# Kernel optimization log

Measured on AMD Instinct MI355X. Metric: run time of the kernel, lower is better.

The kernel has to match this reference:

```python
import jax, jax.numpy as jnp
import numpy as np

N, E, B = 50000, 800000, 512
IN, H, OUT = 128, 64, 32
BN_EPS = 1e-5


def setup_inputs() -> dict:
    key = jax.random.key(0)
    ks = jax.random.split(key, 32)
    inp = {}
    inp["x"] = jax.random.normal(ks[0], (N, IN), dtype=jnp.float32)
    inp["edge_index"] = jax.random.randint(ks[1], (2, E), 0, N, dtype=jnp.int64)
    inp["batch"] = jnp.sort(jax.random.randint(ks[2], (N,), 0, B, dtype=jnp.int64))
    inp["batch_size"] = B
    # GINConv MLP params: Linear(cin,H) -> BN(H) -> ReLU -> Linear(H,H)
    cins = [IN, H, H]
    ki = 3
    for i, cin in enumerate(cins):
        inp[f"c{i}_W1"] = jax.random.normal(ks[ki], (cin, H), dtype=jnp.float32) / np.sqrt(cin); ki += 1
        inp[f"c{i}_b1"] = jnp.zeros((H,), jnp.float32)
        inp[f"c{i}_g1"] = jnp.ones((H,), jnp.float32)
        inp[f"c{i}_bt1"] = jnp.zeros((H,), jnp.float32)
        inp[f"c{i}_W2"] = jax.random.normal(ks[ki], (H, H), dtype=jnp.float32) / np.sqrt(H); ki += 1
        inp[f"c{i}_b2"] = jnp.zeros((H,), jnp.float32)
    # final MLP (norm=None): Linear(H,H) -> ReLU -> [dropout, eval: identity] -> Linear(H,OUT)
    inp["f_W1"] = jax.random.normal(ks[ki], (H, H), dtype=jnp.float32) / np.sqrt(H); ki += 1
    inp["f_b1"] = jnp.zeros((H,), jnp.float32)
    inp["f_W2"] = jax.random.normal(ks[ki], (H, OUT), dtype=jnp.float32) / np.sqrt(H)
    inp["f_b2"] = jnp.zeros((OUT,), jnp.float32)
    return inp


def _bn(h, g, bt):
    # BatchNorm1d, training-mode statistics (biased variance), eps=1e-5
    mean = h.mean(axis=0)
    var = ((h - mean) ** 2).mean(axis=0)
    return g * (h - mean) * jax.lax.rsqrt(var + BN_EPS) + bt


def _gin_conv(x, src, dst, W1, b1, g1, bt1, W2, b2):
    # sum-aggregate neighbor features: agg[i] = sum_{(j->i)} x[j]
    agg = jax.ops.segment_sum(x[src], dst, num_segments=N)  # [N,H_in]
    h = x + agg  # (1+eps)*x + agg, eps=0
    h = jax.nn.relu(_bn(h @ W1 + b1, g1, bt1))
    return h @ W2 + b2


def reference(x, edge_index, batch, batch_size,
              c0_W1, c0_b1, c0_g1, c0_bt1, c0_W2, c0_b2,
              c1_W1, c1_b1, c1_g1, c1_bt1, c1_W2, c1_b2,
              c2_W1, c2_b1, c2_g1, c2_bt1, c2_W2, c2_b2,
              f_W1, f_b1, f_W2, f_b2):
    src, dst = edge_index[0], edge_index[1]
    convs = [(c0_W1, c0_b1, c0_g1, c0_bt1, c0_W2, c0_b2),
             (c1_W1, c1_b1, c1_g1, c1_bt1, c1_W2, c1_b2),
             (c2_W1, c2_b1, c2_g1, c2_bt1, c2_W2, c2_b2)]
    for p in convs:
        x = jax.nn.relu(_gin_conv(x, src, dst, *p))
    # global_add_pool over graph ids
    pooled = jax.ops.segment_sum(x, batch, num_segments=batch_size)  # [B,H]
    h = jax.nn.relu(pooled @ f_W1 + f_b1)  # dropout=0.5 skipped (eval mode)
    return h @ f_W2 + f_b2  # [B,OUT]
```

## Files before the change

### kernel.cpp

```cpp
#include <hip/hip_runtime.h>
#include <hip/hip_fp16.h>

#define NN 50000
#define EE 800000
#define BB 512
#define DIN 128
#define HH 64
#define DOUT 32
#define BN_EPS 1e-5f
#define SCAN_BLOCKS 196
#define GATHER_BLOCKS 2048

template <int CIN>
__global__ __launch_bounds__(256) void proj_kernel(const float* __restrict__ X,
                                                   const float* __restrict__ W,
                                                   __half2* __restrict__ Qh)
{
    __shared__ float sW[CIN * 64];
    __shared__ float sX[16 * CIN];
    const int tid = threadIdx.x;
    const int row0 = blockIdx.x * 16;

    for (int i = tid; i < CIN * 16; i += 256)
        ((float4*)sW)[i] = ((const float4*)W)[i];
    const float* Xb = X + (size_t)row0 * CIN;
    for (int i = tid; i < 16 * CIN / 4; i += 256)
        ((float4*)sX)[i] = ((const float4*)Xb)[i];
    __syncthreads();

    const int col2 = tid & 31;
    const int rg   = tid >> 5;
    float2 acc0 = {0.f, 0.f};
    float2 acc1 = {0.f, 0.f};
    const float* x0p = &sX[(rg * 2 + 0) * CIN];
    const float* x1p = &sX[(rg * 2 + 1) * CIN];
#pragma unroll 4
    for (int k = 0; k < CIN; ++k) {
        const float2 w = *(const float2*)&sW[k * 64 + col2 * 2];
        const float x0 = x0p[k];
        const float x1 = x1p[k];
        acc0.x = fmaf(x0, w.x, acc0.x);
        acc0.y = fmaf(x0, w.y, acc0.y);
        acc1.x = fmaf(x1, w.x, acc1.x);
        acc1.y = fmaf(x1, w.y, acc1.y);
    }
    const int r0 = row0 + rg * 2;
    Qh[(size_t)(r0 + 0) * 32 + col2] = __floats2half2_rn(acc0.x, acc0.y);
    Qh[(size_t)(r0 + 1) * 32 + col2] = __floats2half2_rn(acc1.x, acc1.y);
}

__global__ __launch_bounds__(256) void hist_rank_kernel(const int* __restrict__ dst,
                                                        int* __restrict__ deg,
                                                        unsigned short* __restrict__ rank)
{
    const int e = blockIdx.x * 256 + threadIdx.x;
    rank[e] = (unsigned short)atomicAdd(&deg[dst[e]], 1);
}

__global__ __launch_bounds__(256) void scanA_kernel(const int* __restrict__ deg,
                                                    int* __restrict__ offs,
                                                    int* __restrict__ blockSums)
{
    __shared__ int s[256];
    const int t = threadIdx.x;
    const int i = blockIdx.x * 256 + t;
    const int v = (i < NN) ? deg[i] : 0;
    s[t] = v;
    __syncthreads();
    for (int off = 1; off < 256; off <<= 1) {
        const int a = (t >= off) ? s[t - off] : 0;
        __syncthreads();
        s[t] += a;
        __syncthreads();
    }
    if (i < NN) offs[i] = s[t] - v;
    if (t == 255) blockSums[blockIdx.x] = s[255];
}

__global__ __launch_bounds__(256) void scanB_kernel(const int* __restrict__ blockSums,
                                                    int* __restrict__ blockOff)
{
    __shared__ int s[256];
    const int t = threadIdx.x;
    const int v = (t < SCAN_BLOCKS) ? blockSums[t] : 0;
    s[t] = v;
    __syncthreads();
    for (int off = 1; off < 256; off <<= 1) {
        const int a = (t >= off) ? s[t - off] : 0;
        __syncthreads();
        s[t] += a;
        __syncthreads();
    }
    if (t < SCAN_BLOCKS) blockOff[t] = s[t] - v;
}

__global__ __launch_bounds__(256) void scanC_kernel(int* __restrict__ offs,
                                                    const int* __restrict__ blockOff,
                                                    float* __restrict__ statsbuf,
                                                    float* __restrict__ pooled,
                                                    unsigned int* __restrict__ qzero)
{
    const int i = blockIdx.x * 256 + threadIdx.x;
    if (i < NN) offs[i] += blockOff[blockIdx.x];
    if (i == 0) offs[NN] = EE;
    if (i < 384) statsbuf[i] = 0.f;
    if (i < BB * 64) pooled[i] = 0.f;
    if (blockIdx.x == 1 && threadIdx.x < 32) qzero[threadIdx.x] = 0u;
}

__global__ __launch_bounds__(256) void scatter_kernel(const int* __restrict__ src,
                                                      const int* __restrict__ dst,
                                                      const unsigned short* __restrict__ rank,
                                                      const int* __restrict__ offs,
                                                      unsigned short* __restrict__ srcSorted)
{
    const int e = blockIdx.x * 256 + threadIdx.x;
    const int pos = offs[dst[e]] + (int)rank[e];
    srcSorted[pos] = (unsigned short)src[e];
}

__global__ __launch_bounds__(256) void gather_kernel(const __half2* __restrict__ Qh,
                                                     const int* __restrict__ offs,
                                                     const unsigned short* __restrict__ srcSorted,
                                                     const float* __restrict__ b1,
                                                     float* __restrict__ Z,
                                                     float* __restrict__ sums,
                                                     float* __restrict__ sumsq)
{
    const int tid  = threadIdx.x;
    const int lane = tid & 63;
    const int wid  = tid >> 6;
    const int colq = lane & 15;
    const int grp  = lane >> 4;
    const uint2* Qr = (const uint2*)Qh;
    const float4 bb = ((const float4*)b1)[colq];

    float sa0 = 0.f, sa1 = 0.f, sa2 = 0.f, sa3 = 0.f;
    float ta0 = 0.f, ta1 = 0.f, ta2 = 0.f, ta3 = 0.f;

    for (int node = blockIdx.x * 4 + wid; node < NN; node += GATHER_BLOCKS * 4) {
        const int o0 = offs[node];
        const int o1 = offs[node + 1];
        float a0 = 0.f, a1 = 0.f, a2 = 0.f, a3 = 0.f;
        int j = o0;
        while (o1 - j > 48) {
            int idx[12];
#pragma unroll
            for (int k = 0; k < 12; ++k) idx[k] = srcSorted[j + k * 4 + grp];
            uint2 r[12];
#pragma unroll
            for (int k = 0; k < 12; ++k) r[k] = Qr[(size_t)idx[k] * 16 + colq];
#pragma unroll
            for (int k = 0; k < 12; ++k) {
                float2 p;
                p = __half22float2(*(const __half2*)&r[k].x); a0 += p.x; a1 += p.y;
                p = __half22float2(*(const __half2*)&r[k].y); a2 += p.x; a3 += p.y;
            }
            j += 48;
        }
        {
            int idx[12];
#pragma unroll
            for (int k = 0; k < 12; ++k) {
                const int p = j + k * 4 + grp;
                const int v = srcSorted[p];
                idx[k] = (p < o1) ? v : NN;
            }
            uint2 r[12];
#pragma unroll
            for (int k = 0; k < 12; ++k) r[k] = Qr[(size_t)idx[k] * 16 + colq];
#pragma unroll
            for (int k = 0; k < 12; ++k) {
                float2 p;
                p = __half22float2(*(const __half2*)&r[k].x); a0 += p.x; a1 += p.y;
                p = __half22float2(*(const __half2*)&r[k].y); a2 += p.x; a3 += p.y;
            }
        }
        a0 += __shfl_xor(a0, 16); a1 += __shfl_xor(a1, 16);
        a2 += __shfl_xor(a2, 16); a3 += __shfl_xor(a3, 16);
        a0 += __shfl_xor(a0, 32); a1 += __shfl_xor(a1, 32);
        a2 += __shfl_xor(a2, 32); a3 += __shfl_xor(a3, 32);
        if (grp == 0) {
            const uint2 sr = Qr[(size_t)node * 16 + colq];
            float2 p;
            p = __half22float2(*(const __half2*)&sr.x); a0 += p.x + bb.x; a1 += p.y + bb.y;
            p = __half22float2(*(const __half2*)&sr.y); a2 += p.x + bb.z; a3 += p.y + bb.w;
            float4 zv = {a0, a1, a2, a3};
            ((float4*)Z)[(size_t)node * 16 + colq] = zv;
            sa0 += a0; sa1 += a1; sa2 += a2; sa3 += a3;
            ta0 += a0 * a0; ta1 += a1 * a1; ta2 += a2 * a2; ta3 += a3 * a3;
        }
    }

    __shared__ float red[4][16][8];
    if (grp == 0) {
        float* rp = red[wid][colq];
        rp[0] = sa0; rp[1] = sa1; rp[2] = sa2; rp[3] = sa3;
        rp[4] = ta0; rp[5] = ta1; rp[6] = ta2; rp[7] = ta3;
    }
    __syncthreads();
    if (tid < 128) {
        const int cq = tid >> 3;
        const int k  = tid & 7;
        const float v = red[0][cq][k] + red[1][cq][k] + red[2][cq][k] + red[3][cq][k];
        float* dstp = (k < 4) ? &sums[cq * 4 + k] : &sumsq[cq * 4 + (k - 4)];
        atomicAdd(dstp, v);
    }
}

template <bool POOL>
__global__ __launch_bounds__(256) void gemm2_kernel(const float* __restrict__ Z,
                                                    const float* __restrict__ sums,
                                                    const float* __restrict__ sumsq,
                                                    const float* __restrict__ g1,
                                                    const float* __restrict__ bt1,
                                                    const float* __restrict__ W2,
                                                    const float* __restrict__ b2,
                                                    const int* __restrict__ batch,
                                                    float* __restrict__ out)
{
    __shared__ float sW[64 * 64];
    __shared__ float sH[16 * 64];
    __shared__ float sScale[64];
    __shared__ float sShift[64];
    const int tid = threadIdx.x;
    const int row0 = blockIdx.x * 16;

    if (tid < 64) {
        const float inv_n = 1.0f / (float)NN;
        const float mean = sums[tid] * inv_n;
        const float var = fmaxf(sumsq[tid] * inv_n - mean * mean, 0.f);
        const float sc = g1[tid] * rsqrtf(var + BN_EPS);
        sScale[tid] = sc;
        sShift[tid] = bt1[tid] - mean * sc;
    }
    for (int i = tid; i < 64 * 16; i += 256)
        ((float4*)sW)[i] = ((const float4*)W2)[i];
    __syncthreads();

    const float4* Zb = (const float4*)(Z + (size_t)row0 * 64);
    {
        const int i = tid;
        const float4 z = Zb[i];
        const int c4 = i & 15;
        const float4 sc = ((const float4*)sScale)[c4];
        const float4 sh = ((const float4*)sShift)[c4];
        float4 h;
        h.x = fmaxf(fmaf(z.x, sc.x, sh.x), 0.f);
        h.y = fmaxf(fmaf(z.y, sc.y, sh.y), 0.f);
        h.z = fmaxf(fmaf(z.z, sc.z, sh.z), 0.f);
        h.w = fmaxf(fmaf(z.w, sc.w, sh.w), 0.f);
        ((float4*)sH)[i] = h;
    }
    __syncthreads();

    const int col = tid & 63;
    const int r0  = tid >> 6;
    const float bc = b2[col];
    float acc[4] = {bc, bc, bc, bc};
    for (int k = 0; k < 64; k += 4) {
        const float w0 = sW[(k + 0) * 64 + col];
        const float w1 = sW[(k + 1) * 64 + col];
        const float w2 = sW[(k + 2) * 64 + col];
        const float w3 = sW[(k + 3) * 64 + col];
#pragma unroll
        for (int rr = 0; rr < 4; ++rr) {
            const float4 hv = *(const float4*)&sH[(r0 + rr * 4) * 64 + k];
            acc[rr] = fmaf(hv.x, w0, acc[rr]);
            acc[rr] = fmaf(hv.y, w1, acc[rr]);
            acc[rr] = fmaf(hv.z, w2, acc[rr]);
            acc[rr] = fmaf(hv.w, w3, acc[rr]);
        }
    }
#pragma unroll
    for (int rr = 0; rr < 4; ++rr) {
        const int row = row0 + r0 + rr * 4;
        const float v = fmaxf(acc[rr], 0.f);
        if (POOL) {
            atomicAdd(&out[(size_t)batch[row] * 64 + col], v);
        } else {
            out[(size_t)row * 64 + col] = v;
        }
    }
}

__global__ __launch_bounds__(256) void final_mlp(const float* __restrict__ P,
                                                 const float* __restrict__ W1,
                                                 const float* __restrict__ b1,
                                                 const float* __restrict__ W2,
                                                 const float* __restrict__ b2,
                                                 float* __restrict__ out)
{
    __shared__ float sW1[64 * 64];
    __shared__ float sW2[64 * 32];
    __shared__ float sH[4 * 64];
    const int tid = threadIdx.x;
    const int row0 = blockIdx.x * 4;

    for (int i = tid; i < 1024; i += 256) ((float4*)sW1)[i] = ((const float4*)W1)[i];
    for (int i = tid; i < 512; i += 256) ((float4*)sW2)[i] = ((const float4*)W2)[i];
    __syncthreads();

    const int col = tid & 63;
    const int r = tid >> 6;
    float acc = b1[col];
    const float* prow = P + (size_t)(row0 + r) * 64;
    for (int k = 0; k < 64; ++k) acc = fmaf(prow[k], sW1[k * 64 + col], acc);
    sH[r * 64 + col] = fmaxf(acc, 0.f);
    __syncthreads();

    if (tid < 128) {
        const int c = tid & 31;
        const int r2 = tid >> 5;
        float a2 = b2[c];
        for (int k = 0; k < 64; ++k) a2 = fmaf(sH[r2 * 64 + k], sW2[k * 32 + c], a2);
        out[(size_t)(row0 + r2) * 32 + c] = a2;
    }
}

extern "C" void kernel_launch(void* const* d_in, const int* in_sizes, int n_in,
                              void* d_out, int out_size, void* d_ws, size_t ws_size,
                              hipStream_t stream)
{
    const float* x   = (const float*)d_in[0];
    const int* ei    = (const int*)d_in[1];
    const int* batch = (const int*)d_in[2];
    const float* cW1[3] = {(const float*)d_in[4],  (const float*)d_in[10], (const float*)d_in[16]};
    const float* cb1[3] = {(const float*)d_in[5],  (const float*)d_in[11], (const float*)d_in[17]};
    const float* cg1[3] = {(const float*)d_in[6],  (const float*)d_in[12], (const float*)d_in[18]};
    const float* cbt[3] = {(const float*)d_in[7],  (const float*)d_in[13], (const float*)d_in[19]};
    const float* cW2[3] = {(const float*)d_in[8],  (const float*)d_in[14], (const float*)d_in[20]};
    const float* cb2[3] = {(const float*)d_in[9],  (const float*)d_in[15], (const float*)d_in[21]};
    const float* fW1 = (const float*)d_in[22];
    const float* fb1 = (const float*)d_in[23];
    const float* fW2 = (const float*)d_in[24];
    const float* fb2 = (const float*)d_in[25];
    float* out = (float*)d_out;

    float* bufX     = (float*)d_ws;
    __half2* Qh     = (__half2*)(bufX + (size_t)NN * 64);
    float* pooled   = (float*)(Qh + (size_t)(NN + 1) * 32);
    float* statsbuf = pooled + (size_t)BB * 64;
    int* deg        = (int*)(statsbuf + 384);
    int* offs       = deg + NN;
    int* blockSums  = offs + (NN + 1);
    int* blockOff   = blockSums + 256;
    unsigned short* rank      = (unsigned short*)(blockOff + 256);
    unsigned short* srcSorted = rank + EE;

    const int* esrc = ei;
    const int* edst = ei + EE;

    const int gemm_blocks = NN / 16;
    const int edge_blocks = EE / 256;

    hipMemsetAsync(deg, 0, NN * sizeof(int), stream);
    hist_rank_kernel<<<edge_blocks, 256, 0, stream>>>(edst, deg, rank);
    scanA_kernel<<<SCAN_BLOCKS, 256, 0, stream>>>(deg, offs, blockSums);
    scanB_kernel<<<1, 256, 0, stream>>>(blockSums, blockOff);
    scanC_kernel<<<SCAN_BLOCKS, 256, 0, stream>>>(offs, blockOff, statsbuf, pooled,
                                                  (unsigned int*)(Qh + (size_t)NN * 32));
    scatter_kernel<<<edge_blocks, 256, 0, stream>>>(esrc, edst, rank, offs, srcSorted);

    for (int layer = 0; layer < 3; ++layer) {
        float* sums  = statsbuf + layer * 128;
        float* sumsq = sums + 64;

        if (layer == 0)
            proj_kernel<DIN><<<gemm_blocks, 256, 0, stream>>>(x, cW1[0], Qh);
        else
            proj_kernel<HH><<<gemm_blocks, 256, 0, stream>>>(bufX, cW1[layer], Qh);

        gather_kernel<<<GATHER_BLOCKS, 256, 0, stream>>>(Qh, offs, srcSorted, cb1[layer],
                                                         bufX, sums, sumsq);

        if (layer < 2) {
            gemm2_kernel<false><<<gemm_blocks, 256, 0, stream>>>(bufX, sums, sumsq, cg1[layer],
                                                                 cbt[layer], cW2[layer], cb2[layer],
                                                                 nullptr, bufX);
        } else {
            gemm2_kernel<true><<<gemm_blocks, 256, 0, stream>>>(bufX, sums, sumsq, cg1[layer],
                                                                cbt[layer], cW2[layer], cb2[layer],
                                                                batch, pooled);
        }
    }

    final_mlp<<<BB / 4, 256, 0, stream>>>(pooled, fW1, fb1, fW2, fb2, out);
}
```

Measured before the change: 382.4 us.

## Pad CSR neighbor lists to multiples of sixteen for branch-free vectorized gather

Each node's neighbor list is padded to at least 16 entries, rounded up to a multiple of 16, and filled with a sentinel index that points to a zeroed Q row. This lets the gather load indices as aligned uint4 vectors and drop the per-element bounds checks. The gather is also remapped so each wave handles a node with two 32-lane halves, each lane covering one half2 column. The cost is a larger index buffer, an extra fill kernel, and wasted gathers on padding entries for low-degree nodes.

```diff
diff --git a/kernel.cpp b/kernel.cpp
--- a/kernel.cpp
+++ b/kernel.cpp
@@ -10,6 +10,7 @@
 #define BN_EPS 1e-5f
 #define SCAN_BLOCKS 196
 #define GATHER_BLOCKS 2048
+#define PADMAX (16 * NN + EE + 64)
 
 template <int CIN>
 __global__ __launch_bounds__(256) void proj_kernel(const float* __restrict__ X,
@@ -49,6 +50,12 @@
     Qh[(size_t)(r0 + 1) * 32 + col2] = __floats2half2_rn(acc1.x, acc1.y);
 }
 
+__global__ __launch_bounds__(256) void fill_kernel(unsigned int* __restrict__ dstw)
+{
+    const int i = blockIdx.x * 256 + threadIdx.x;
+    if (i < PADMAX / 2) dstw[i] = 0xC350C350u;
+}
+
 __global__ __launch_bounds__(256) void hist_rank_kernel(const int* __restrict__ dst,
                                                         int* __restrict__ deg,
                                                         unsigned short* __restrict__ rank)
@@ -58,13 +65,17 @@
 }
 
 __global__ __launch_bounds__(256) void scanA_kernel(const int* __restrict__ deg,
-                                                    int* __restrict__ offs,
+                                                    int* __restrict__ poffs,
                                                     int* __restrict__ blockSums)
 {
     __shared__ int s[256];
     const int t = threadIdx.x;
     const int i = blockIdx.x * 256 + t;
-    const int v = (i < NN) ? deg[i] : 0;
+    int v = 0;
+    if (i < NN) {
+        const int d = deg[i];
+        v = (d <= 16) ? 16 : ((d + 15) & ~15);
+    }
     s[t] = v;
     __syncthreads();
     for (int off = 1; off < 256; off <<= 1) {
@@ -73,12 +84,13 @@
         s[t] += a;
         __syncthreads();
     }
-    if (i < NN) offs[i] = s[t] - v;
+    if (i < NN) poffs[i] = s[t] - v;
     if (t == 255) blockSums[blockIdx.x] = s[255];
 }
 
 __global__ __launch_bounds__(256) void scanB_kernel(const int* __restrict__ blockSums,
-                                                    int* __restrict__ blockOff)
+                                                    int* __restrict__ blockOff,
+                                                    int* __restrict__ poffs)
 {
     __shared__ int s[256];
     const int t = threadIdx.x;
@@ -92,17 +104,17 @@
         __syncthreads();
     }
     if (t < SCAN_BLOCKS) blockOff[t] = s[t] - v;
-}
-
-__global__ __launch_bounds__(256) void scanC_kernel(int* __restrict__ offs,
+    if (t == SCAN_BLOCKS - 1) poffs[NN] = s[t];
+}
+
+__global__ __launch_bounds__(256) void scanC_kernel(int* __restrict__ poffs,
                                                     const int* __restrict__ blockOff,
                                                     float* __restrict__ statsbuf,
                                                     float* __restrict__ pooled,
                                                     unsigned int* __restrict__ qzero)
 {
     const int i = blockIdx.x * 256 + threadIdx.x;
-    if (i < NN) offs[i] += blockOff[blockIdx.x];
-    if (i == 0) offs[NN] = EE;
+    if (i < NN) poffs[i] += blockOff[blockIdx.x];
     if (i < 384) statsbuf[i] = 0.f;
     if (i < BB * 64) pooled[i] = 0.f;
     if (blockIdx.x == 1 && threadIdx.x < 32) qzero[threadIdx.x] = 0u;
@@ -111,99 +123,122 @@
 __global__ __launch_bounds__(256) void scatter_kernel(const int* __restrict__ src,
                                                       const int* __restrict__ dst,
                                                       const unsigned short* __restrict__ rank,
-                                                      const int* __restrict__ offs,
-                                                      unsigned short* __restrict__ srcSorted)
+                                                      const int* __restrict__ poffs,
+                                                      unsigned short* __restrict__ srcPadded)
 {
     const int e = blockIdx.x * 256 + threadIdx.x;
-    const int pos = offs[dst[e]] + (int)rank[e];
-    srcSorted[pos] = (unsigned short)src[e];
+    const int pos = poffs[dst[e]] + (int)rank[e];
+    srcPadded[pos] = (unsigned short)src[e];
 }
 
 __global__ __launch_bounds__(256) void gather_kernel(const __half2* __restrict__ Qh,
-                                                     const int* __restrict__ offs,
-                                                     const unsigned short* __restrict__ srcSorted,
+                                                     const int* __restrict__ poffs,
+                                                     const unsigned short* __restrict__ srcPadded,
                                                      const float* __restrict__ b1,
                                                      float* __restrict__ Z,
                                                      float* __restrict__ sums,
                                                      float* __restrict__ sumsq)
 {
-    const int tid  = threadIdx.x;
-    const int lane = tid & 63;
-    const int wid  = tid >> 6;
-    const int colq = lane & 15;
-    const int grp  = lane >> 4;
-    const uint2* Qr = (const uint2*)Qh;
-    const float4 bb = ((const float4*)b1)[colq];
-
-    float sa0 = 0.f, sa1 = 0.f, sa2 = 0.f, sa3 = 0.f;
-    float ta0 = 0.f, ta1 = 0.f, ta2 = 0.f, ta3 = 0.f;
+    const int tid   = threadIdx.x;
+    const int lane  = tid & 63;
+    const int wid   = tid >> 6;
+    const int c     = lane & 31;
+    const int grp   = lane >> 5;
+    const int shamt = grp << 4;
+    const uint* Qd  = (const uint*)Qh;
+    const float2 bb = ((const float2*)b1)[c];
+
+    float2 sa = {0.f, 0.f};
+    float2 ta = {0.f, 0.f};
 
     for (int node = blockIdx.x * 4 + wid; node < NN; node += GATHER_BLOCKS * 4) {
-        const int o0 = offs[node];
-        const int o1 = offs[node + 1];
-        float a0 = 0.f, a1 = 0.f, a2 = 0.f, a3 = 0.f;
-        int j = o0;
-        while (o1 - j > 48) {
-            int idx[12];
-#pragma unroll
-            for (int k = 0; k < 12; ++k) idx[k] = srcSorted[j + k * 4 + grp];
-            uint2 r[12];
-#pragma unroll
-            for (int k = 0; k < 12; ++k) r[k] = Qr[(size_t)idx[k] * 16 + colq];
-#pragma unroll
-            for (int k = 0; k < 12; ++k) {
-                float2 p;
-                p = __half22float2(*(const __half2*)&r[k].x); a0 += p.x; a1 += p.y;
-                p = __half22float2(*(const __half2*)&r[k].y); a2 += p.x; a3 += p.y;
+        const int p0 = poffs[node];
+        const int p1 = poffs[node + 1];
+        const bool two = (p1 - p0) > 16;
+
+        const uint4 ia = *(const uint4*)(srcPadded + p0);
+        const uint4 ib = *(const uint4*)(srcPadded + p0 + 8);
+        uint4 ia2, ib2;
+        if (two) {
+            ia2 = *(const uint4*)(srcPadded + p0 + 16);
+            ib2 = *(const uint4*)(srcPadded + p0 + 24);
+        }
+        const uint sr = Qd[(size_t)node * 32 + c];
+
+        uint r[16];
+#pragma unroll
+        for (int k = 0; k < 4; ++k) {
+            r[k]     = Qd[(size_t)(((&ia.x)[k] >> shamt) & 0xffffu) * 32 + c];
+            r[4 + k] = Qd[(size_t)(((&ib.x)[k] >> shamt) & 0xffffu) * 32 + c];
+        }
+        if (two) {
+#pragma unroll
+            for (int k = 0; k < 4; ++k) {
+                r[8 + k]  = Qd[(size_t)(((&ia2.x)[k] >> shamt) & 0xffffu) * 32 + c];
+                r[12 + k] = Qd[(size_t)(((&ib2.x)[k] >> shamt) & 0xffffu) * 32 + c];
             }
-            j += 48;
-        }
-        {
-            int idx[12];
-#pragma unroll
-            for (int k = 0; k < 12; ++k) {
-                const int p = j + k * 4 + grp;
-                const int v = srcSorted[p];
-                idx[k] = (p < o1) ? v : NN;
+        }
+
+        float2 acc = {0.f, 0.f};
+#pragma unroll
+        for (int k = 0; k < 8; ++k) {
+            const float2 p = __half22float2(*(const __half2*)&r[k]);
+            acc.x += p.x;
+            acc.y += p.y;
+        }
+        if (two) {
+#pragma unroll
+            for (int k = 8; k < 16; ++k) {
+                const float2 p = __half22float2(*(const __half2*)&r[k]);
+                acc.x += p.x;
+                acc.y += p.y;
             }
-            uint2 r[12];
-#pragma unroll
-            for (int k = 0; k < 12; ++k) r[k] = Qr[(size_t)idx[k] * 16 + colq];
-#pragma unroll
-            for (int k = 0; k < 12; ++k) {
-                float2 p;
-                p = __half22float2(*(const __half2*)&r[k].x); a0 += p.x; a1 += p.y;
-                p = __half22float2(*(const __half2*)&r[k].y); a2 += p.x; a3 += p.y;
+        }
+        for (int j = p0 + 32; j < p1; j += 16) {
+            const uint4 ja = *(const uint4*)(srcPadded + j);
+            const uint4 jb = *(const uint4*)(srcPadded + j + 8);
+            uint rr[8];
+#pragma unroll
+            for (int k = 0; k < 4; ++k) {
+                rr[k]     = Qd[(size_t)(((&ja.x)[k] >> shamt) & 0xffffu) * 32 + c];
+                rr[4 + k] = Qd[(size_t)(((&jb.x)[k] >> shamt) & 0xffffu) * 32 + c];
             }
-        }
-        a0 += __shfl_xor(a0, 16); a1 += __shfl_xor(a1, 16);
-        a2 += __shfl_xor(a2, 16); a3 += __shfl_xor(a3, 16);
-        a0 += __shfl_xor(a0, 32); a1 += __shfl_xor(a1, 32);
-        a2 += __shfl_xor(a2, 32); a3 += __shfl_xor(a3, 32);
+#pragma unroll
+            for (int k = 0; k < 8; ++k) {
+                const float2 p = __half22float2(*(const __half2*)&rr[k]);
+                acc.x += p.x;
+                acc.y += p.y;
+            }
+        }
+
+        acc.x += __shfl_xor(acc.x, 32);
+        acc.y += __shfl_xor(acc.y, 32);
+
         if (grp == 0) {
-            const uint2 sr = Qr[(size_t)node * 16 + colq];
-            float2 p;
-            p = __half22float2(*(const __half2*)&sr.x); a0 += p.x + bb.x; a1 += p.y + bb.y;
-            p = __half22float2(*(const __half2*)&sr.y); a2 += p.x + bb.z; a3 += p.y + bb.w;
-            float4 zv = {a0, a1, a2, a3};
-            ((float4*)Z)[(size_t)node * 16 + colq] = zv;
-            sa0 += a0; sa1 += a1; sa2 += a2; sa3 += a3;
-            ta0 += a0 * a0; ta1 += a1 * a1; ta2 += a2 * a2; ta3 += a3 * a3;
-        }
-    }
-
-    __shared__ float red[4][16][8];
+            const float2 p = __half22float2(*(const __half2*)&sr);
+            acc.x += p.x + bb.x;
+            acc.y += p.y + bb.y;
+            ((float2*)Z)[(size_t)node * 32 + c] = acc;
+            sa.x += acc.x; sa.y += acc.y;
+            ta.x += acc.x * acc.x; ta.y += acc.y * acc.y;
+        }
+    }
+
+    __shared__ float red[4][32][4];
     if (grp == 0) {
-        float* rp = red[wid][colq];
-        rp[0] = sa0; rp[1] = sa1; rp[2] = sa2; rp[3] = sa3;
-        rp[4] = ta0; rp[5] = ta1; rp[6] = ta2; rp[7] = ta3;
+        float* rp = red[wid][c];
+        rp[0] = sa.x; rp[1] = sa.y; rp[2] = ta.x; rp[3] = ta.y;
     }
     __syncthreads();
     if (tid < 128) {
-        const int cq = tid >> 3;
-        const int k  = tid & 7;
-        const float v = red[0][cq][k] + red[1][cq][k] + red[2][cq][k] + red[3][cq][k];
-        float* dstp = (k < 4) ? &sums[cq * 4 + k] : &sumsq[cq * 4 + (k - 4)];
+        const int c2 = tid >> 2;
+        const int k  = tid & 3;
+        const float v = red[0][c2][k] + red[1][c2][k] + red[2][c2][k] + red[3][c2][k];
+        float* dstp;
+        if (k == 0)      dstp = &sums[2 * c2 + 0];
+        else if (k == 1) dstp = &sums[2 * c2 + 1];
+        else if (k == 2) dstp = &sumsq[2 * c2 + 0];
+        else             dstp = &sumsq[2 * c2 + 1];
         atomicAdd(dstp, v);
     }
 }
@@ -342,11 +377,12 @@
     float* pooled   = (float*)(Qh + (size_t)(NN + 1) * 32);
     float* statsbuf = pooled + (size_t)BB * 64;
     int* deg        = (int*)(statsbuf + 384);
-    int* offs       = deg + NN;
-    int* blockSums  = offs + (NN + 1);
+    int* poffs      = deg + NN;
+    int* blockSums  = poffs + (NN + 1);
     int* blockOff   = blockSums + 256;
-    unsigned short* rank      = (unsigned short*)(blockOff + 256);
-    unsigned short* srcSorted = rank + EE;
+    uintptr_t pa = ((uintptr_t)(blockOff + 256) + 15) & ~(uintptr_t)15;
+    unsigned short* srcPadded = (unsigned short*)pa;
+    unsigned short* rank      = srcPadded + PADMAX;
 
     const int* esrc = ei;
     const int* edst = ei + EE;
@@ -355,12 +391,13 @@
     const int edge_blocks = EE / 256;
 
     hipMemsetAsync(deg, 0, NN * sizeof(int), stream);
+    fill_kernel<<<(PADMAX / 2 + 255) / 256, 256, 0, stream>>>((unsigned int*)srcPadded);
     hist_rank_kernel<<<edge_blocks, 256, 0, stream>>>(edst, deg, rank);
-    scanA_kernel<<<SCAN_BLOCKS, 256, 0, stream>>>(deg, offs, blockSums);
-    scanB_kernel<<<1, 256, 0, stream>>>(blockSums, blockOff);
-    scanC_kernel<<<SCAN_BLOCKS, 256, 0, stream>>>(offs, blockOff, statsbuf, pooled,
+    scanA_kernel<<<SCAN_BLOCKS, 256, 0, stream>>>(deg, poffs, blockSums);
+    scanB_kernel<<<1, 256, 0, stream>>>(blockSums, blockOff, poffs);
+    scanC_kernel<<<SCAN_BLOCKS, 256, 0, stream>>>(poffs, blockOff, statsbuf, pooled,
                                                   (unsigned int*)(Qh + (size_t)NN * 32));
-    scatter_kernel<<<edge_blocks, 256, 0, stream>>>(esrc, edst, rank, offs, srcSorted);
+    scatter_kernel<<<edge_blocks, 256, 0, stream>>>(esrc, edst, rank, poffs, srcPadded);
 
     for (int layer = 0; layer < 3; ++layer) {
         float* sums  = statsbuf + layer * 128;
@@ -371,7 +408,7 @@
         else
             proj_kernel<HH><<<gemm_blocks, 256, 0, stream>>>(bufX, cW1[layer], Qh);
 
-        gather_kernel<<<GATHER_BLOCKS, 256, 0, stream>>>(Qh, offs, srcSorted, cb1[layer],
+        gather_kernel<<<GATHER_BLOCKS, 256, 0, stream>>>(Qh, poffs, srcPadded, cb1[layer],
                                                          bufX, sums, sumsq);
 
         if (layer < 2) {
```

New measurement: 365.1 us. -4.5%, faster.
